# Kernel tuning notes

Hardware: AMD Instinct MI355X
Metric: run time of the kernel (lower is better)

## Reference

```python
import jax, jax.numpy as jnp
import numpy as np

IN_FEATURES = 4096
OUT_FEATURES = 4096
BATCH = 8192


def setup_inputs() -> dict:
    key = jax.random.key(0)
    k1, k2 = jax.random.split(key)
    x = jax.random.normal(k1, (BATCH, IN_FEATURES), dtype=jnp.float32)
    # nn.init.normal_(vals, std=1/sqrt(in_features))
    vals = jax.random.normal(k2, (IN_FEATURES + OUT_FEATURES - 1,), dtype=jnp.float32) / np.sqrt(IN_FEATURES)
    return {"x": x, "vals": vals}


def _build_weight(vals):
    # W[i, j] = vals[(out_features - 1 - i) + j]  -> constant diagonals (Toeplitz)
    idx = jnp.arange(IN_FEATURES)                      # [in]
    row_offsets = jnp.arange(OUT_FEATURES - 1, -1, -1)  # [out], descending
    indices = row_offsets[:, None] + idx[None, :]       # [out, in]
    return vals[indices]


def reference(x, vals):
    W = _build_weight(vals)          # [out, in]
    return x @ W.T                   # [B, out]
```

## Files before the change

kernel.cpp:

```cpp
#include <hip/hip_runtime.h>
#include <stdint.h>

#define MM 8192
#define NN 4096
#define KK 4096
#define BM 256
#define BN 256
#define BK 64
#define NT (KK / BK)

typedef __attribute__((ext_vector_type(8))) short short8;
typedef __attribute__((ext_vector_type(4))) float floatx4;
typedef int int4a __attribute__((ext_vector_type(4), aligned(4)));

__device__ inline unsigned short f2bf(float f) {
    unsigned int u = __float_as_uint(f);
    u += 0x7FFFu + ((u >> 16) & 1u);
    return (unsigned short)(u >> 16);
}

__global__ void prep_x_kernel(const float* __restrict__ x, unsigned short* __restrict__ xb) {
    size_t i = (size_t)blockIdx.x * 256 + threadIdx.x;
    const float4* x4 = (const float4*)x;
    float4 v0 = x4[i * 2];
    float4 v1 = x4[i * 2 + 1];
    ushort4 o0, o1;
    o0.x = f2bf(v0.x); o0.y = f2bf(v0.y); o0.z = f2bf(v0.z); o0.w = f2bf(v0.w);
    o1.x = f2bf(v1.x); o1.y = f2bf(v1.y); o1.z = f2bf(v1.z); o1.w = f2bf(v1.w);
    *(ushort4*)(xb + i * 8)     = o0;
    *(ushort4*)(xb + i * 8 + 4) = o1;
}

__global__ void prep_vals_kernel(const float* __restrict__ vals,
                                 unsigned short* __restrict__ vlo,
                                 unsigned short* __restrict__ vhi) {
    int i = blockIdx.x * 256 + threadIdx.x;
    if (i < KK + NN - 1) {
        unsigned short s = f2bf(vals[i]);
        vlo[i] = s;
        if (i > 0) vhi[i - 1] = s;
    }
}

#define GLOAD_LDS16(g, l)                                              \
    __builtin_amdgcn_global_load_lds(                                  \
        (__attribute__((address_space(1))) void*)(g),                  \
        (__attribute__((address_space(3))) void*)(l), 16, 0, 0)

__global__ __launch_bounds__(512, 2) void gemm_kernel(
        const unsigned short* __restrict__ A,
        const unsigned short* __restrict__ vlo,
        const unsigned short* __restrict__ vhi,
        float* __restrict__ C) {
    __shared__ unsigned short ldsA[4][BM * BK];

    const int tid  = threadIdx.x;
    const int lane = tid & 63;
    const int w    = tid >> 6;
    const int n0 = blockIdx.x * BN;
    const int m0 = blockIdx.y * BM;

    const int quad = lane >> 4;
    const int l16  = lane & 15;
    const int wm   = (w >> 2) * 128;
    const int wn   = (w & 3) * 64;

    const int lr8 = lane >> 3;
    const int cg  = (lane & 7) ^ (lr8 & 7);
    const unsigned short* aSrc = A + (size_t)(m0 + w * 32 + lr8) * KK + cg * 8;
    const int sBase = (w * 32) * BK;

    const unsigned short* bptr[4];
#pragma unroll
    for (int j = 0; j < 4; ++j) {
        int idx0 = (NN - 1) - (n0 + wn + l16) - j * 16 + quad * 8;
        bptr[j] = (idx0 & 1) ? (vhi + (idx0 - 1)) : (vlo + idx0);
    }

    floatx4 acc[8][4] = {};
    short8 b0r[8], b1r[8];

#define STAGE1(BI, T, G)                                               \
    GLOAD_LDS16(aSrc + (size_t)(G) * 8 * KK + (size_t)(T) * BK,        \
                &ldsA[BI][sBase + (G) * 8 * BK])

#define LOADB(DST, T)                                                  \
    do {                                                               \
        _Pragma("unroll")                                              \
        for (int j = 0; j < 4; ++j) {                                  \
            _Pragma("unroll")                                          \
            for (int kh = 0; kh < 2; ++kh) {                           \
                int4a t_ = *(const int4a*)(bptr[j] + (size_t)(T) * BK + kh * 32); \
                __builtin_memcpy(&(DST)[j * 2 + kh], &t_, 16);         \
            }                                                          \
        }                                                              \
    } while (0)

#define AFRAG(AF, BI, P)                                               \
    do {                                                               \
        _Pragma("unroll")                                              \
        for (int ii = 0; ii < 2; ++ii) {                               \
            _Pragma("unroll")                                          \
            for (int kh = 0; kh < 2; ++kh)                             \
                (AF)[ii * 2 + kh] = *(const short8*)&ldsA[BI][         \
                    (wm + (2 * (P) + ii) * 16 + l16) * BK +            \
                    (((kh * 4 + quad) ^ (l16 & 7)) * 8)];              \
        }                                                              \
    } while (0)

#define MFMA16(AF, BS, P)                                              \
    do {                                                               \
        _Pragma("unroll")                                              \
        for (int kh = 0; kh < 2; ++kh) {                               \
            _Pragma("unroll")                                          \
            for (int ii = 0; ii < 2; ++ii) {                           \
                _Pragma("unroll")                                      \
                for (int j = 0; j < 4; ++j)                            \
                    acc[2 * (P) + ii][j] =                             \
                        __builtin_amdgcn_mfma_f32_16x16x32_bf16(       \
                            (AF)[ii * 2 + kh], (BS)[j * 2 + kh],       \
                            acc[2 * (P) + ii][j], 0, 0, 0);            \
            }                                                          \
        }                                                              \
    } while (0)

#define SB()    __builtin_amdgcn_s_barrier()
#define PRIO(x) __builtin_amdgcn_s_setprio(x)
#define WAITV(N) asm volatile("s_waitcnt vmcnt(" #N ")" ::: "memory")

#pragma unroll
    for (int g = 0; g < 4; ++g) STAGE1(0, 0, g);
    LOADB(b0r, 0);
#pragma unroll
    for (int g = 0; g < 4; ++g) STAGE1(1, 1, g);
    WAITV(12);
    SB();

#define TILE(BI, T, BCUR, BNXT, DOB, DOST, LW)                         \
    do {                                                               \
        short8 af_[4];                                                 \
        AFRAG(af_, BI, 0);                                             \
        if (DOB) LOADB(BNXT, (T) + 1);                                 \
        if (DOST) STAGE1(((BI) + 2) & 3, (T) + 2, 0);                  \
        SB(); PRIO(1); MFMA16(af_, BCUR, 0); PRIO(0); SB();            \
        AFRAG(af_, BI, 1);                                             \
        if (DOST) STAGE1(((BI) + 2) & 3, (T) + 2, 1);                  \
        SB(); PRIO(1); MFMA16(af_, BCUR, 1); PRIO(0); SB();            \
        AFRAG(af_, BI, 2);                                             \
        if (DOST) STAGE1(((BI) + 2) & 3, (T) + 2, 2);                  \
        SB(); PRIO(1); MFMA16(af_, BCUR, 2); PRIO(0); SB();            \
        AFRAG(af_, BI, 3);                                             \
        if (DOST) STAGE1(((BI) + 2) & 3, (T) + 2, 3);                  \
        SB(); PRIO(1); MFMA16(af_, BCUR, 3); PRIO(0);                  \
        LW; SB();                                                      \
    } while (0)

    for (int u = 0; u < 15; ++u) {
        const int t = u * 4;
        TILE(0, t + 0, b0r, b1r, 1, 1, WAITV(12));
        TILE(1, t + 1, b1r, b0r, 1, 1, WAITV(12));
        TILE(2, t + 2, b0r, b1r, 1, 1, WAITV(12));
        TILE(3, t + 3, b1r, b0r, 1, 1, WAITV(12));
    }
    TILE(0, 60, b0r, b1r, 1, 1, WAITV(12));
    TILE(1, 61, b1r, b0r, 1, 1, WAITV(12));
    TILE(2, 62, b0r, b1r, 1, 0, WAITV(8));
    TILE(3, 63, b1r, b0r, 0, 0, (void)0);

    float* cW = C + (size_t)(m0 + wm) * NN + (n0 + wn);
#pragma unroll
    for (int i = 0; i < 8; ++i) {
#pragma unroll
        for (int j = 0; j < 4; ++j) {
            float* cp = cW + (size_t)(i * 16 + quad * 4) * NN + j * 16 + l16;
#pragma unroll
            for (int r = 0; r < 4; ++r)
                cp[(size_t)r * NN] = acc[i][j][r];
        }
    }
#undef TILE
#undef STAGE1
#undef LOADB
#undef AFRAG
#undef MFMA16
}

extern "C" void kernel_launch(void* const* d_in, const int* in_sizes, int n_in,
                              void* d_out, int out_size, void* d_ws, size_t ws_size,
                              hipStream_t stream) {
    const float* x    = (const float*)d_in[0];
    const float* vals = (const float*)d_in[1];
    float* out = (float*)d_out;

    unsigned short* xb  = (unsigned short*)d_ws;
    unsigned short* vlo = xb + (size_t)MM * KK;
    unsigned short* vhi = vlo + 16384;

    prep_x_kernel<<<MM * KK / 8 / 256, 256, 0, stream>>>(x, xb);
    prep_vals_kernel<<<(KK + NN - 1 + 255) / 256, 256, 0, stream>>>(vals, vlo, vhi);

    dim3 grid(NN / BN, MM / BM);
    gemm_kernel<<<grid, 512, 0, stream>>>(xb, vlo, vhi, out);
}
```

Before: 469.8 us.

## Double-buffer A fragments in registers and cut per-tile barriers to one

Replaces the four barrier pairs per K tile with a single barrier placed before reading the next LDS buffer. A fragments are double-buffered in two register sets (afA/afB), so LDS reads for the next sub-step overlap the MFMAs of the current one. Empty asm memory clobbers around the barrier keep the compiler from moving LDS accesses across it. The cost is higher VGPR pressure and a looser wave lockstep, which leans on the 4-deep LDS ring for correctness.

```diff
diff --git a/kernel.cpp b/kernel.cpp
--- a/kernel.cpp
+++ b/kernel.cpp
@@ -79,6 +79,7 @@
 
     floatx4 acc[8][4] = {};
     short8 b0r[8], b1r[8];
+    short8 afA[4], afB[4];
 
 #define STAGE1(BI, T, G)                                               \
     GLOAD_LDS16(aSrc + (size_t)(G) * 8 * KK + (size_t)(T) * BK,        \
@@ -124,7 +125,12 @@
         }                                                              \
     } while (0)
 
-#define SB()    __builtin_amdgcn_s_barrier()
+#define SB()                                                           \
+    do {                                                               \
+        asm volatile("" ::: "memory");                                 \
+        __builtin_amdgcn_s_barrier();                                  \
+        asm volatile("" ::: "memory");                                 \
+    } while (0)
 #define PRIO(x) __builtin_amdgcn_s_setprio(x)
 #define WAITV(N) asm volatile("s_waitcnt vmcnt(" #N ")" ::: "memory")
 
@@ -135,37 +141,37 @@
     for (int g = 0; g < 4; ++g) STAGE1(1, 1, g);
     WAITV(12);
     SB();
-
-#define TILE(BI, T, BCUR, BNXT, DOB, DOST, LW)                         \
-    do {                                                               \
-        short8 af_[4];                                                 \
-        AFRAG(af_, BI, 0);                                             \
+    AFRAG(afA, 0, 0);
+
+#define TILE(BI, T, BCUR, BNXT, DOB, DOST, DONXT, LW)                  \
+    do {                                                               \
         if (DOB) LOADB(BNXT, (T) + 1);                                 \
+        AFRAG(afB, BI, 1);                                             \
         if (DOST) STAGE1(((BI) + 2) & 3, (T) + 2, 0);                  \
-        SB(); PRIO(1); MFMA16(af_, BCUR, 0); PRIO(0); SB();            \
-        AFRAG(af_, BI, 1);                                             \
+        PRIO(1); MFMA16(afA, BCUR, 0); PRIO(0);                        \
+        AFRAG(afA, BI, 2);                                             \
         if (DOST) STAGE1(((BI) + 2) & 3, (T) + 2, 1);                  \
-        SB(); PRIO(1); MFMA16(af_, BCUR, 1); PRIO(0); SB();            \
-        AFRAG(af_, BI, 2);                                             \
+        PRIO(1); MFMA16(afB, BCUR, 1); PRIO(0);                        \
+        AFRAG(afB, BI, 3);                                             \
         if (DOST) STAGE1(((BI) + 2) & 3, (T) + 2, 2);                  \
-        SB(); PRIO(1); MFMA16(af_, BCUR, 2); PRIO(0); SB();            \
-        AFRAG(af_, BI, 3);                                             \
+        PRIO(1); MFMA16(afA, BCUR, 2); PRIO(0);                        \
         if (DOST) STAGE1(((BI) + 2) & 3, (T) + 2, 3);                  \
-        SB(); PRIO(1); MFMA16(af_, BCUR, 3); PRIO(0);                  \
-        LW; SB();                                                      \
+        LW;                                                            \
+        if (DONXT) { SB(); AFRAG(afA, ((BI) + 1) & 3, 0); }            \
+        PRIO(1); MFMA16(afB, BCUR, 3); PRIO(0);                        \
     } while (0)
 
     for (int u = 0; u < 15; ++u) {
         const int t = u * 4;
-        TILE(0, t + 0, b0r, b1r, 1, 1, WAITV(12));
-        TILE(1, t + 1, b1r, b0r, 1, 1, WAITV(12));
-        TILE(2, t + 2, b0r, b1r, 1, 1, WAITV(12));
-        TILE(3, t + 3, b1r, b0r, 1, 1, WAITV(12));
-    }
-    TILE(0, 60, b0r, b1r, 1, 1, WAITV(12));
-    TILE(1, 61, b1r, b0r, 1, 1, WAITV(12));
-    TILE(2, 62, b0r, b1r, 1, 0, WAITV(8));
-    TILE(3, 63, b1r, b0r, 0, 0, (void)0);
+        TILE(0, t + 0, b0r, b1r, 1, 1, 1, WAITV(12));
+        TILE(1, t + 1, b1r, b0r, 1, 1, 1, WAITV(12));
+        TILE(2, t + 2, b0r, b1r, 1, 1, 1, WAITV(12));
+        TILE(3, t + 3, b1r, b0r, 1, 1, 1, WAITV(12));
+    }
+    TILE(0, 60, b0r, b1r, 1, 1, 1, WAITV(12));
+    TILE(1, 61, b1r, b0r, 1, 1, 1, WAITV(12));
+    TILE(2, 62, b0r, b1r, 1, 0, 1, WAITV(8));
+    TILE(3, 63, b1r, b0r, 0, 0, 0, (void)0);
 
     float* cW = C + (size_t)(m0 + wm) * NN + (n0 + wn);
 #pragma unroll
```

After: 453.7 us. -3.4%, faster.
